# Performance work log

Measured on AMD Instinct MI355X. Metric: run time of the kernel, lower is better.

## Reference

```python
import jax, jax.numpy as jnp
import numpy as np

EPS = 1e-8  # torch CosineSimilarity default eps

def setup_inputs() -> dict:
    key = jax.random.key(0)
    kv, kt, k1, k2, k3, k4 = jax.random.split(key, 6)
    B, S = 16, 1024
    VD, TD, H = 1024, 768, 512
    visual_features = jax.random.normal(kv, (B, S, VD), dtype=jnp.float32)
    text_features = jax.random.normal(kt, (B, S, TD), dtype=jnp.float32)
    # nn.Linear params: weight [out, in], bias [out]
    Wv = jax.random.normal(k1, (H, VD), dtype=jnp.float32) * (1.0 / np.sqrt(VD))
    bv = jax.random.normal(k2, (H,), dtype=jnp.float32) * 0.01
    Wt = jax.random.normal(k3, (H, TD), dtype=jnp.float32) * (1.0 / np.sqrt(TD))
    bt = jax.random.normal(k4, (H,), dtype=jnp.float32) * 0.01
    return {"visual_features": visual_features, "text_features": text_features,
            "Wv": Wv, "bv": bv, "Wt": Wt, "bt": bt}

def reference(visual_features, text_features, Wv, bv, Wt, bt):
    # Linear projections
    v = jnp.einsum('bsd,hd->bsh', visual_features, Wv) + bv  # [B,S,H]
    t = jnp.einsum('bsd,hd->bsh', text_features, Wt) + bt    # [B,S,H]
    # Cosine similarity matrix via normalized batched GEMM
    # (algebraically equal to broadcasting CosineSimilarity over (B,S,S,H))
    dots = jnp.einsum('bih,bjh->bij', v, t)                   # [B,S,S]
    vn = jnp.linalg.norm(v, axis=-1)                          # [B,S]
    tn = jnp.linalg.norm(t, axis=-1)                          # [B,S]
    denom = jnp.maximum(vn[:, :, None] * tn[:, None, :], EPS)
    return dots / denom
```

## Files before the change

### kernel.cpp

```cpp
#include <hip/hip_runtime.h>
#include <hip/hip_bf16.h>

typedef __bf16 bf16x8 __attribute__((ext_vector_type(8)));
typedef __bf16 bf16x4 __attribute__((ext_vector_type(4)));
typedef float  f32x4  __attribute__((ext_vector_type(4)));

#define MFMA16(a, b, c) __builtin_amdgcn_mfma_f32_16x16x32_bf16((a), (b), (c), 0, 0, 0)

#define BATCH 16
#define SEQ   1024
#define VD    1024
#define TD    768
#define HDIM  512
#define MROWS (BATCH * SEQ)

typedef __attribute__((address_space(1))) const unsigned int gas_uint;
typedef __attribute__((address_space(3))) unsigned int las_uint;

__device__ __forceinline__ void async_copy16(const void* g, void* l) {
    __builtin_amdgcn_global_load_lds((gas_uint*)g, (las_uint*)l, 16, 0, 0);
}

__device__ __forceinline__ void stage_tile256(const __bf16* __restrict__ src,
                                              size_t ld, int row0, int k0,
                                              __bf16* __restrict__ buf, int tid) {
#pragma unroll
    for (int i = 0; i < 4; ++i) {
        const int c = i * 512 + tid;
        const int r = c >> 3;
        const int g = (c & 7) ^ (r & 7);
        async_copy16(&src[(size_t)(row0 + r) * ld + k0 + g * 8],
                     &buf[(c & ~63) * 8]);
    }
}

__device__ __forceinline__ bf16x8 frag_read(const __bf16* __restrict__ buf,
                                            int r, int h, int fq) {
    return *reinterpret_cast<const bf16x8*>(&buf[(r * 8 + ((h * 4 + fq) ^ (r & 7))) * 8]);
}

__device__ __forceinline__ void ldA_chunk(const float* __restrict__ src, int K,
                                          int row0, int k0, int tid, int i,
                                          float4* regs) {
    const int c = i * 512 + tid;
    const int r = c >> 3;
    const int j = c & 7;
    const float4* p = reinterpret_cast<const float4*>(src) +
                      (size_t)(row0 + r) * (K >> 2) + (k0 >> 2) + j * 2;
    regs[i * 2]     = p[0];
    regs[i * 2 + 1] = p[1];
}

__device__ __forceinline__ void stA_chunk(__bf16* __restrict__ buf, int tid,
                                          int i, const float4* regs) {
    const int c = i * 512 + tid;
    const int r = c >> 3;
    const int j = c & 7;
    const float4 x0 = regs[i * 2], x1 = regs[i * 2 + 1];
    bf16x8 q = {(__bf16)x0.x, (__bf16)x0.y, (__bf16)x0.z, (__bf16)x0.w,
                (__bf16)x1.x, (__bf16)x1.y, (__bf16)x1.z, (__bf16)x1.w};
    *reinterpret_cast<bf16x8*>(&buf[(r * 8 + (j ^ (r & 7))) * 8]) = q;
}

#define NC_WV (HDIM * VD / 4)
#define NC_WT (HDIM * TD / 4)
#define NW_PAIRS ((NC_WV + NC_WT) / 2)
#define CONVW_BLOCKS (NW_PAIRS / 256)
#define NZ_BLOCKS (2 * MROWS / 4 / 256)
#define CONVW_GRID (CONVW_BLOCKS + NZ_BLOCKS)

__global__ __launch_bounds__(256) void conv_w_kernel(
    const float* __restrict__ Wv, const float* __restrict__ Wt,
    __bf16* __restrict__ Wvb, __bf16* __restrict__ Wtb,
    float* __restrict__ n2z) {
    const int blk = blockIdx.x;
    if (blk >= CONVW_BLOCKS) {
        const int zi = (blk - CONVW_BLOCKS) * 256 + threadIdx.x;
        reinterpret_cast<float4*>(n2z)[zi] = float4{0.f, 0.f, 0.f, 0.f};
        return;
    }
    int k = (blk * 256 + threadIdx.x) * 2;
    const float* src;
    __bf16* dst;
    if (k < NC_WV) { src = Wv; dst = Wvb; }
    else { k -= NC_WV; src = Wt; dst = Wtb; }
    const float4 x0 = reinterpret_cast<const float4*>(src)[k];
    const float4 x1 = reinterpret_cast<const float4*>(src)[k + 1];
    bf16x8 q = {(__bf16)x0.x, (__bf16)x0.y, (__bf16)x0.z, (__bf16)x0.w,
                (__bf16)x1.x, (__bf16)x1.y, (__bf16)x1.z, (__bf16)x1.w};
    reinterpret_cast<bf16x8*>(dst)[k >> 1] = q;
}

__global__ __launch_bounds__(512, 2) void proj_kernel(
    const float* __restrict__ Xv32, const __bf16* __restrict__ Wvb, const float* __restrict__ bv_,
    const float* __restrict__ Xt32, const __bf16* __restrict__ Wtb, const float* __restrict__ bt_,
    __bf16* __restrict__ vout, __bf16* __restrict__ tout,
    float* __restrict__ vn2, float* __restrict__ tn2)
{
    __shared__ __bf16 As[3][256 * 64];
    __shared__ __bf16 Bs[2][256 * 64];

    const int L  = blockIdx.x;
    const int x  = L & 7;
    const int s  = L >> 3;
    const int z  = s >> 4;
    const int ss = s & 15;
    const int m0 = (x * 8 + (ss >> 1)) * 256;
    const int n0 = (ss & 1) * 256;

    const float* X; const __bf16* Wb; const float* bias; __bf16* out; float* n2; int K;
    if (z == 0) { X = Xv32; Wb = Wvb; bias = bv_; out = vout; n2 = vn2; K = VD; }
    else        { X = Xt32; Wb = Wtb; bias = bt_; out = tout; n2 = tn2; K = TD; }

    const int tid  = threadIdx.x;
    const int lane = tid & 63;
    const int wave = tid >> 6;
    const int wr   = wave >> 2;
    const int wc   = wave & 3;
    const int fr   = lane & 15;
    const int fq   = lane >> 4;

    f32x4 acc[8][4] = {};
    const int NKT = K >> 6;

    float4 regs[8];
    {
        float4 rA0[8];
        ldA_chunk(X, K, m0, 0, tid, 0, rA0);
        ldA_chunk(X, K, m0, 0, tid, 1, rA0);
        ldA_chunk(X, K, m0, 0, tid, 2, rA0);
        ldA_chunk(X, K, m0, 0, tid, 3, rA0);
        stage_tile256(Wb, K, n0, 0,  Bs[0], tid);
        stage_tile256(Wb, K, n0, 64, Bs[1], tid);
        stA_chunk(As[0], tid, 0, rA0);
        stA_chunk(As[0], tid, 1, rA0);
        stA_chunk(As[0], tid, 2, rA0);
        stA_chunk(As[0], tid, 3, rA0);
        if (1 < NKT) {
            ldA_chunk(X, K, m0, 64, tid, 0, regs);
            ldA_chunk(X, K, m0, 64, tid, 1, regs);
            ldA_chunk(X, K, m0, 64, tid, 2, regs);
            ldA_chunk(X, K, m0, 64, tid, 3, regs);
        }
        asm volatile("s_waitcnt vmcnt(12)" ::: "memory");
        asm volatile("s_waitcnt lgkmcnt(0)" ::: "memory");
        __builtin_amdgcn_s_barrier();
    }

    int ar = 0, aw = 1;
    for (int kt = 0; kt < NKT; ++kt) {
        const __bf16* Ab = As[ar];
        const __bf16* Bb = Bs[kt & 1];
        const int doW = (kt + 1 < NKT);
        const int doL = (kt + 2 < NKT);
        bf16x8 bfr[4][2];
#pragma unroll
        for (int q = 0; q < 4; ++q) {
            bf16x8 afr[2][2];
#pragma unroll
            for (int m2 = 0; m2 < 2; ++m2)
#pragma unroll
                for (int h = 0; h < 2; ++h)
                    afr[m2][h] = frag_read(Ab, wr * 128 + (q * 2 + m2) * 16 + fr, h, fq);
            if (q == 0) {
#pragma unroll
                for (int n = 0; n < 4; ++n)
#pragma unroll
                    for (int h = 0; h < 2; ++h)
                        bfr[n][h] = frag_read(Bb, wc * 64 + n * 16 + fr, h, fq);
            }
            if (doW) stA_chunk(As[aw], tid, q, regs);
            if (doL) ldA_chunk(X, K, m0, (kt + 2) << 6, tid, q, regs);
            __builtin_amdgcn_s_setprio(1);
#pragma unroll
            for (int h = 0; h < 2; ++h)
#pragma unroll
                for (int m2 = 0; m2 < 2; ++m2)
#pragma unroll
                    for (int n = 0; n < 4; ++n)
                        acc[q * 2 + m2][n] = MFMA16(afr[m2][h], bfr[n][h], acc[q * 2 + m2][n]);
            __builtin_amdgcn_s_setprio(0);
        }
        if (kt < NKT - 1) {
            __builtin_amdgcn_s_barrier();
            __builtin_amdgcn_sched_barrier(0);
            if (kt + 2 < NKT) {
                stage_tile256(Wb, K, n0, (kt + 2) << 6, Bs[kt & 1], tid);
                asm volatile("s_waitcnt vmcnt(12)" ::: "memory");
            } else {
                asm volatile("s_waitcnt vmcnt(0)" ::: "memory");
            }
            asm volatile("s_waitcnt lgkmcnt(0)" ::: "memory");
            __builtin_amdgcn_sched_barrier(0);
            __builtin_amdgcn_s_barrier();
            ar = aw;
            aw = (aw == 2) ? 0 : aw + 1;
        }
    }

    float bc[4];
#pragma unroll
    for (int n = 0; n < 4; ++n)
        bc[n] = bias[n0 + wc * 64 + n * 16 + fr];

#pragma unroll
    for (int mf = 0; mf < 8; ++mf) {
        const int rowb = m0 + wr * 128 + mf * 16 + fq * 4;
#pragma unroll
        for (int r = 0; r < 4; ++r) {
            float s_ = 0.f;
#pragma unroll
            for (int n = 0; n < 4; ++n) {
                const float e = acc[mf][n][r] + bc[n];
                out[(size_t)(rowb + r) * HDIM + n0 + wc * 64 + n * 16 + fr] = (__bf16)e;
                s_ = fmaf(e, e, s_);
            }
            s_ += __shfl_xor(s_, 1);
            s_ += __shfl_xor(s_, 2);
            s_ += __shfl_xor(s_, 4);
            s_ += __shfl_xor(s_, 8);
            if (fr == 0) atomicAdd(&n2[rowb + r], s_);
        }
    }
}

__global__ __launch_bounds__(512, 2) void dots_kernel(const __bf16* __restrict__ v,
                                                      const __bf16* __restrict__ t,
                                                      const float* __restrict__ vn2,
                                                      const float* __restrict__ tn2,
                                                      float* __restrict__ out) {
    __shared__ __bf16 As[2][256 * 64];
    __shared__ __bf16 Bs[2][256 * 64];

    const int L  = blockIdx.x;
    const int x  = L & 7;
    const int s  = L >> 3;
    const int b  = x * 2 + (s >> 4);
    const int i0 = ((s >> 2) & 3) * 256;
    const int j0 = (s & 3) * 256;

    const __bf16* vb = v + (size_t)b * SEQ * HDIM;
    const __bf16* tb = t + (size_t)b * SEQ * HDIM;

    const int tid  = threadIdx.x;
    const int lane = tid & 63;
    const int wave = tid >> 6;
    const int wr   = wave >> 2;
    const int wc   = wave & 3;
    const int fr   = lane & 15;
    const int fq   = lane >> 4;

    f32x4 acc[8][4] = {};
    const int NKT = HDIM >> 6;

    stage_tile256(vb, HDIM, i0, 0,  As[0], tid);
    stage_tile256(tb, HDIM, j0, 0,  Bs[0], tid);
    stage_tile256(vb, HDIM, i0, 64, As[1], tid);
    stage_tile256(tb, HDIM, j0, 64, Bs[1], tid);
    asm volatile("s_waitcnt vmcnt(8)" ::: "memory");
    __builtin_amdgcn_s_barrier();

    for (int kt = 0; kt < NKT; ++kt) {
        const __bf16* Ab = As[kt & 1];
        const __bf16* Bb = Bs[kt & 1];
        bf16x8 bfr[4][2];
#pragma unroll
        for (int q = 0; q < 4; ++q) {
            bf16x8 afr[2][2];
#pragma unroll
            for (int m2 = 0; m2 < 2; ++m2)
#pragma unroll
                for (int h = 0; h < 2; ++h)
                    afr[m2][h] = frag_read(Ab, wr * 128 + (q * 2 + m2) * 16 + fr, h, fq);
            if (q == 0) {
#pragma unroll
                for (int n = 0; n < 4; ++n)
#pragma unroll
                    for (int h = 0; h < 2; ++h)
                        bfr[n][h] = frag_read(Bb, wc * 64 + n * 16 + fr, h, fq);
            }
            __builtin_amdgcn_s_barrier();
            __builtin_amdgcn_s_setprio(1);
#pragma unroll
            for (int h = 0; h < 2; ++h)
#pragma unroll
                for (int m2 = 0; m2 < 2; ++m2)
#pragma unroll
                    for (int n = 0; n < 4; ++n)
                        acc[q * 2 + m2][n] = MFMA16(afr[m2][h], bfr[n][h], acc[q * 2 + m2][n]);
            __builtin_amdgcn_s_setprio(0);
        }
        if (kt < NKT - 1) {
            __builtin_amdgcn_s_barrier();
            __builtin_amdgcn_sched_barrier(0);
            if (kt + 2 < NKT) {
                const int kk = (kt + 2) << 6;
                stage_tile256(vb, HDIM, i0, kk, As[kt & 1], tid);
                stage_tile256(tb, HDIM, j0, kk, Bs[kt & 1], tid);
                asm volatile("s_waitcnt vmcnt(8)" ::: "memory");
            } else {
                asm volatile("s_waitcnt vmcnt(0)" ::: "memory");
            }
            __builtin_amdgcn_sched_barrier(0);
            __builtin_amdgcn_s_barrier();
        }
    }

    float vr2[8][4];
#pragma unroll
    for (int mf = 0; mf < 8; ++mf)
#pragma unroll
        for (int r = 0; r < 4; ++r)
            vr2[mf][r] = vn2[b * SEQ + i0 + wr * 128 + mf * 16 + fq * 4 + r];

    float* outb = out + ((size_t)b << 20);
#pragma unroll
    for (int n = 0; n < 4; ++n) {
        const int j     = j0 + wc * 64 + n * 16 + fr;
        const float tj2 = tn2[b * SEQ + j];
#pragma unroll
        for (int mf = 0; mf < 8; ++mf) {
            const int ib = i0 + wr * 128 + mf * 16 + fq * 4;
#pragma unroll
            for (int r = 0; r < 4; ++r) {
                const float denom = fmaxf(sqrtf(vr2[mf][r] * tj2), 1e-8f);
                outb[(size_t)(ib + r) * SEQ + j] = acc[mf][n][r] * __builtin_amdgcn_rcpf(denom);
            }
        }
    }
}

extern "C" void kernel_launch(void* const* d_in, const int* in_sizes, int n_in,
                              void* d_out, int out_size, void* d_ws, size_t ws_size,
                              hipStream_t stream) {
    const float* Xv = (const float*)d_in[0];
    const float* Xt = (const float*)d_in[1];
    const float* Wv = (const float*)d_in[2];
    const float* bv = (const float*)d_in[3];
    const float* Wt = (const float*)d_in[4];
    const float* bt = (const float*)d_in[5];
    float* out = (float*)d_out;

    char* ws = (char*)d_ws;
    size_t off = 0;
    __bf16* v   = (__bf16*)(ws + off); off += (size_t)MROWS * HDIM * 2;
    __bf16* t   = (__bf16*)(ws + off); off += (size_t)MROWS * HDIM * 2;
    __bf16* Wvb = (__bf16*)(ws + off); off += (size_t)HDIM * VD * 2;
    __bf16* Wtb = (__bf16*)(ws + off); off += (size_t)HDIM * TD * 2;
    float*  vn2 = (float*)(ws + off);  off += (size_t)MROWS * 4;
    float*  tn2 = (float*)(ws + off);  off += (size_t)MROWS * 4;

    conv_w_kernel<<<CONVW_GRID, 256, 0, stream>>>(Wv, Wt, Wvb, Wtb, vn2);

    proj_kernel<<<256, 512, 0, stream>>>(Xv, Wvb, bv, Xt, Wtb, bt, v, t, vn2, tn2);

    dots_kernel<<<256, 512, 0, stream>>>(v, t, vn2, tn2, out);
}
```

Measured before the change: 222.8 us.

## Shrink projection GEMM tiles to 128x128 with 256-thread blocks and more blocks

The projection kernel moves from 256x256 tiles with 512 threads and 256 blocks to 128x128 tiles with 256 threads and 1024 blocks. The A-buffer ring drops from triple to double buffering. The aim is better occupancy and load balance across the CUs by launching more, smaller blocks. The cost is lower data reuse per tile, which roughly doubles global reads of X and W per output element.

```diff
diff --git a/kernel.cpp b/kernel.cpp
--- a/kernel.cpp
+++ b/kernel.cpp
@@ -34,32 +34,45 @@
     }
 }
 
+__device__ __forceinline__ void stage_tile128(const __bf16* __restrict__ src,
+                                              size_t ld, int row0, int k0,
+                                              __bf16* __restrict__ buf, int tid) {
+#pragma unroll
+    for (int i = 0; i < 4; ++i) {
+        const int c = i * 256 + tid;
+        const int r = c >> 3;
+        const int g = (c & 7) ^ (r & 7);
+        async_copy16(&src[(size_t)(row0 + r) * ld + k0 + g * 8],
+                     &buf[(c & ~63) * 8]);
+    }
+}
+
 __device__ __forceinline__ bf16x8 frag_read(const __bf16* __restrict__ buf,
                                             int r, int h, int fq) {
     return *reinterpret_cast<const bf16x8*>(&buf[(r * 8 + ((h * 4 + fq) ^ (r & 7))) * 8]);
 }
 
-__device__ __forceinline__ void ldA_chunk(const float* __restrict__ src, int K,
-                                          int row0, int k0, int tid, int i,
-                                          float4* regs) {
-    const int c = i * 512 + tid;
+__device__ __forceinline__ void ldA_chunk128(const float* __restrict__ src, int K,
+                                             int row0, int k0, int tid, int q,
+                                             float4* regs) {
+    const int c = q * 256 + tid;
     const int r = c >> 3;
     const int j = c & 7;
     const float4* p = reinterpret_cast<const float4*>(src) +
                       (size_t)(row0 + r) * (K >> 2) + (k0 >> 2) + j * 2;
-    regs[i * 2]     = p[0];
-    regs[i * 2 + 1] = p[1];
-}
-
-__device__ __forceinline__ void stA_chunk(__bf16* __restrict__ buf, int tid,
-                                          int i, const float4* regs) {
-    const int c = i * 512 + tid;
+    regs[q * 2]     = p[0];
+    regs[q * 2 + 1] = p[1];
+}
+
+__device__ __forceinline__ void stA_chunk128(__bf16* __restrict__ buf, int tid,
+                                             int q, const float4* regs) {
+    const int c = q * 256 + tid;
     const int r = c >> 3;
     const int j = c & 7;
-    const float4 x0 = regs[i * 2], x1 = regs[i * 2 + 1];
-    bf16x8 q = {(__bf16)x0.x, (__bf16)x0.y, (__bf16)x0.z, (__bf16)x0.w,
+    const float4 x0 = regs[q * 2], x1 = regs[q * 2 + 1];
+    bf16x8 w = {(__bf16)x0.x, (__bf16)x0.y, (__bf16)x0.z, (__bf16)x0.w,
                 (__bf16)x1.x, (__bf16)x1.y, (__bf16)x1.z, (__bf16)x1.w};
-    *reinterpret_cast<bf16x8*>(&buf[(r * 8 + (j ^ (r & 7))) * 8]) = q;
+    *reinterpret_cast<bf16x8*>(&buf[(r * 8 + (j ^ (r & 7))) * 8]) = w;
 }
 
 #define NC_WV (HDIM * VD / 4)
@@ -91,22 +104,22 @@
     reinterpret_cast<bf16x8*>(dst)[k >> 1] = q;
 }
 
-__global__ __launch_bounds__(512, 2) void proj_kernel(
+__global__ __launch_bounds__(256, 2) void proj_kernel(
     const float* __restrict__ Xv32, const __bf16* __restrict__ Wvb, const float* __restrict__ bv_,
     const float* __restrict__ Xt32, const __bf16* __restrict__ Wtb, const float* __restrict__ bt_,
     __bf16* __restrict__ vout, __bf16* __restrict__ tout,
     float* __restrict__ vn2, float* __restrict__ tn2)
 {
-    __shared__ __bf16 As[3][256 * 64];
-    __shared__ __bf16 Bs[2][256 * 64];
+    __shared__ __bf16 As[2][128 * 64];
+    __shared__ __bf16 Bs[2][128 * 64];
 
     const int L  = blockIdx.x;
     const int x  = L & 7;
     const int s  = L >> 3;
-    const int z  = s >> 4;
-    const int ss = s & 15;
-    const int m0 = (x * 8 + (ss >> 1)) * 256;
-    const int n0 = (ss & 1) * 256;
+    const int z  = s >> 6;
+    const int ss = s & 63;
+    const int m0 = (x * 16 + (ss >> 2)) * 128;
+    const int n0 = (ss & 3) * 128;
 
     const float* X; const __bf16* Wb; const float* bias; __bf16* out; float* n2; int K;
     if (z == 0) { X = Xv32; Wb = Wvb; bias = bv_; out = vout; n2 = vn2; K = VD; }
@@ -115,53 +128,50 @@
     const int tid  = threadIdx.x;
     const int lane = tid & 63;
     const int wave = tid >> 6;
-    const int wr   = wave >> 2;
-    const int wc   = wave & 3;
+    const int wr   = wave >> 1;
+    const int wc   = wave & 1;
     const int fr   = lane & 15;
     const int fq   = lane >> 4;
 
-    f32x4 acc[8][4] = {};
+    f32x4 acc[4][4] = {};
     const int NKT = K >> 6;
 
     float4 regs[8];
     {
         float4 rA0[8];
-        ldA_chunk(X, K, m0, 0, tid, 0, rA0);
-        ldA_chunk(X, K, m0, 0, tid, 1, rA0);
-        ldA_chunk(X, K, m0, 0, tid, 2, rA0);
-        ldA_chunk(X, K, m0, 0, tid, 3, rA0);
-        stage_tile256(Wb, K, n0, 0,  Bs[0], tid);
-        stage_tile256(Wb, K, n0, 64, Bs[1], tid);
-        stA_chunk(As[0], tid, 0, rA0);
-        stA_chunk(As[0], tid, 1, rA0);
-        stA_chunk(As[0], tid, 2, rA0);
-        stA_chunk(As[0], tid, 3, rA0);
+        ldA_chunk128(X, K, m0, 0, tid, 0, rA0);
+        ldA_chunk128(X, K, m0, 0, tid, 1, rA0);
+        ldA_chunk128(X, K, m0, 0, tid, 2, rA0);
+        ldA_chunk128(X, K, m0, 0, tid, 3, rA0);
+        stage_tile128(Wb, K, n0, 0,  Bs[0], tid);
+        stage_tile128(Wb, K, n0, 64, Bs[1], tid);
+        stA_chunk128(As[0], tid, 0, rA0);
+        stA_chunk128(As[0], tid, 1, rA0);
+        stA_chunk128(As[0], tid, 2, rA0);
+        stA_chunk128(As[0], tid, 3, rA0);
         if (1 < NKT) {
-            ldA_chunk(X, K, m0, 64, tid, 0, regs);
-            ldA_chunk(X, K, m0, 64, tid, 1, regs);
-            ldA_chunk(X, K, m0, 64, tid, 2, regs);
-            ldA_chunk(X, K, m0, 64, tid, 3, regs);
+            ldA_chunk128(X, K, m0, 64, tid, 0, regs);
+            ldA_chunk128(X, K, m0, 64, tid, 1, regs);
+            ldA_chunk128(X, K, m0, 64, tid, 2, regs);
+            ldA_chunk128(X, K, m0, 64, tid, 3, regs);
         }
         asm volatile("s_waitcnt vmcnt(12)" ::: "memory");
         asm volatile("s_waitcnt lgkmcnt(0)" ::: "memory");
         __builtin_amdgcn_s_barrier();
     }
 
-    int ar = 0, aw = 1;
     for (int kt = 0; kt < NKT; ++kt) {
-        const __bf16* Ab = As[ar];
+        const __bf16* Ab = As[kt & 1];
         const __bf16* Bb = Bs[kt & 1];
         const int doW = (kt + 1 < NKT);
         const int doL = (kt + 2 < NKT);
         bf16x8 bfr[4][2];
 #pragma unroll
         for (int q = 0; q < 4; ++q) {
-            bf16x8 afr[2][2];
-#pragma unroll
-            for (int m2 = 0; m2 < 2; ++m2)
-#pragma unroll
-                for (int h = 0; h < 2; ++h)
-                    afr[m2][h] = frag_read(Ab, wr * 128 + (q * 2 + m2) * 16 + fr, h, fq);
+            bf16x8 afr[2];
+#pragma unroll
+            for (int h = 0; h < 2; ++h)
+                afr[h] = frag_read(Ab, wr * 64 + q * 16 + fr, h, fq);
             if (q == 0) {
 #pragma unroll
                 for (int n = 0; n < 4; ++n)
@@ -169,23 +179,21 @@
                     for (int h = 0; h < 2; ++h)
                         bfr[n][h] = frag_read(Bb, wc * 64 + n * 16 + fr, h, fq);
             }
-            if (doW) stA_chunk(As[aw], tid, q, regs);
-            if (doL) ldA_chunk(X, K, m0, (kt + 2) << 6, tid, q, regs);
+            if (doW) stA_chunk128(As[(kt + 1) & 1], tid, q, regs);
+            if (doL) ldA_chunk128(X, K, m0, (kt + 2) << 6, tid, q, regs);
             __builtin_amdgcn_s_setprio(1);
 #pragma unroll
             for (int h = 0; h < 2; ++h)
 #pragma unroll
-                for (int m2 = 0; m2 < 2; ++m2)
-#pragma unroll
-                    for (int n = 0; n < 4; ++n)
-                        acc[q * 2 + m2][n] = MFMA16(afr[m2][h], bfr[n][h], acc[q * 2 + m2][n]);
+                for (int n = 0; n < 4; ++n)
+                    acc[q][n] = MFMA16(afr[h], bfr[n][h], acc[q][n]);
             __builtin_amdgcn_s_setprio(0);
         }
         if (kt < NKT - 1) {
             __builtin_amdgcn_s_barrier();
             __builtin_amdgcn_sched_barrier(0);
             if (kt + 2 < NKT) {
-                stage_tile256(Wb, K, n0, (kt + 2) << 6, Bs[kt & 1], tid);
+                stage_tile128(Wb, K, n0, (kt + 2) << 6, Bs[kt & 1], tid);
                 asm volatile("s_waitcnt vmcnt(12)" ::: "memory");
             } else {
                 asm volatile("s_waitcnt vmcnt(0)" ::: "memory");
@@ -193,8 +201,6 @@
             asm volatile("s_waitcnt lgkmcnt(0)" ::: "memory");
             __builtin_amdgcn_sched_barrier(0);
             __builtin_amdgcn_s_barrier();
-            ar = aw;
-            aw = (aw == 2) ? 0 : aw + 1;
         }
     }
 
@@ -204,8 +210,8 @@
         bc[n] = bias[n0 + wc * 64 + n * 16 + fr];
 
 #pragma unroll
-    for (int mf = 0; mf < 8; ++mf) {
-        const int rowb = m0 + wr * 128 + mf * 16 + fq * 4;
+    for (int mf = 0; mf < 4; ++mf) {
+        const int rowb = m0 + wr * 64 + mf * 16 + fq * 4;
 #pragma unroll
         for (int r = 0; r < 4; ++r) {
             float s_ = 0.f;
@@ -352,7 +358,7 @@
 
     conv_w_kernel<<<CONVW_GRID, 256, 0, stream>>>(Wv, Wt, Wvb, Wtb, vn2);
 
-    proj_kernel<<<256, 512, 0, stream>>>(Xv, Wvb, bv, Xt, Wtb, bt, v, t, vn2, tn2);
+    proj_kernel<<<1024, 256, 0, stream>>>(Xv, Wvb, bv, Xt, Wtb, bt, v, t, vn2, tn2);
 
     dots_kernel<<<256, 512, 0, stream>>>(v, t, vn2, tn2, out);
 }
```

Measured after the change: 233.1 us. 1.05x slower.
